# Optimization experiments

Measured on AMD Instinct MI355X. Metric: run time of the kernel, lower is better.

Reference implementation:

```python
import jax, jax.numpy as jnp
import numpy as np

N = 100_000       # nodes
E = 1_600_000     # directed edges (avg degree 16)
IN, H, Z = 128, 128, 64


def setup_inputs() -> dict:
    key = jax.random.key(0)
    ks = jax.random.split(key, 8)
    x = jax.random.normal(ks[0], (N, IN), dtype=jnp.float32)
    edge_index = jax.random.randint(ks[1], (2, E), 0, N, dtype=jnp.int32)
    # Glorot-ish init like PyG GCNConv
    W1 = jax.random.normal(ks[2], (IN, H), dtype=jnp.float32) / np.sqrt(IN).astype(np.float32)
    b1 = jnp.zeros((H,), dtype=jnp.float32)
    Wmu = jax.random.normal(ks[3], (H, Z), dtype=jnp.float32) / np.sqrt(H).astype(np.float32)
    bmu = jnp.zeros((Z,), dtype=jnp.float32)
    Wlv = jax.random.normal(ks[4], (H, Z), dtype=jnp.float32) / np.sqrt(H).astype(np.float32)
    blv = jnp.zeros((Z,), dtype=jnp.float32)
    return {"x": x, "edge_index": edge_index, "W1": W1, "b1": b1,
            "Wmu": Wmu, "bmu": bmu, "Wlv": Wlv, "blv": blv}


def _gcn_conv(x, src, dst, norm, W, b):
    """PyG GCNConv: out = scatter_add(norm * (x @ W)[src], dst) + b."""
    h = x @ W                                   # [N, out_dim]
    msg = h[src] * norm[:, None]                # [E+N, out_dim] gather + scale
    out = jax.ops.segment_sum(msg, dst, num_segments=N)
    return out + b


def reference(x, edge_index, W1, b1, Wmu, bmu, Wlv, blv):
    loop = jnp.arange(N, dtype=edge_index.dtype)
    src = jnp.concatenate([edge_index[0], loop])   # add self-loops (PyG default)
    dst = jnp.concatenate([edge_index[1], loop])
    # symmetric normalization D^{-1/2} (A+I) D^{-1/2}
    deg = jax.ops.segment_sum(jnp.ones_like(dst, dtype=x.dtype), dst, num_segments=N)
    dinv = jax.lax.rsqrt(deg)                      # deg >= 1 thanks to self-loops
    norm = dinv[src] * dinv[dst]                   # [E+N]
    h = jax.nn.relu(_gcn_conv(x, src, dst, norm, W1, b1))
    mu = _gcn_conv(h, src, dst, norm, Wmu, bmu)
    logvar = _gcn_conv(h, src, dst, norm, Wlv, blv)
    return (mu, logvar)
```

## Files before the change

kernel.cpp:

```cpp
#include <hip/hip_runtime.h>
#include <hip/hip_bf16.h>
#include <stdint.h>

static inline size_t ws_align(size_t x) { return (x + 255) & ~(size_t)255; }

typedef __attribute__((ext_vector_type(8))) short bf16x8;
typedef __attribute__((ext_vector_type(4))) float f32x4;

__device__ __forceinline__ uint32_t pack_bf16(float a, float b) {
    uint32_t ua = __float_as_uint(a), ub = __float_as_uint(b);
    ua = (ua + 0x7fffu + ((ua >> 16) & 1u)) >> 16;
    ub = (ub + 0x7fffu + ((ub >> 16) & 1u)) >> 16;
    return ua | (ub << 16);
}
__device__ __forceinline__ uint16_t cvt_bf16(float a) {
    uint32_t ua = __float_as_uint(a);
    return (uint16_t)((ua + 0x7fffu + ((ua >> 16) & 1u)) >> 16);
}
__device__ __forceinline__ float bf_lo(uint32_t v) { return __uint_as_float(v << 16); }
__device__ __forceinline__ float bf_hi(uint32_t v) { return __uint_as_float(v & 0xffff0000u); }


__global__ __launch_bounds__(256) void k_bcount(const int* __restrict__ dst, int* __restrict__ cntAB,
                                                int E, int nchunk, int NB) {
    __shared__ int h[512];
    for (int t = threadIdx.x; t < NB; t += 256) h[t] = 0;
    __syncthreads();
    const int c = blockIdx.x;
    const int per = (E + nchunk - 1) / nchunk;
    const int e0 = c * per, e1 = (e0 + per < E) ? e0 + per : E;
    for (int e = e0 + threadIdx.x; e < e1; e += 256)
        atomicAdd(&h[dst[e] >> 8], 1);
    __syncthreads();
    for (int t = threadIdx.x; t < NB; t += 256) cntAB[t * nchunk + c] = h[t];
}

__global__ __launch_bounds__(256) void k_bscatter(const int* __restrict__ src, const int* __restrict__ dst,
                                                  const int* __restrict__ baseAB, uint2* __restrict__ ebkt,
                                                  int E, int nchunk, int NB) {
    __shared__ int bump[512];
    const int c = blockIdx.x;
    for (int t = threadIdx.x; t < NB; t += 256) bump[t] = baseAB[t * nchunk + c];
    __syncthreads();
    const int per = (E + nchunk - 1) / nchunk;
    const int e0 = c * per, e1 = (e0 + per < E) ? e0 + per : E;
    for (int e = e0 + threadIdx.x; e < e1; e += 256) {
        int d = dst[e], s = src[e];
        int pos = atomicAdd(&bump[d >> 8], 1);
        ebkt[pos] = make_uint2((uint32_t)s, (uint32_t)d);
    }
}

__global__ __launch_bounds__(256) void k_bhist(const uint2* __restrict__ ebkt, const int* __restrict__ baseAB,
                                               int* __restrict__ cnt, int nchunk, int N) {
    __shared__ int h[256];
    h[threadIdx.x] = 0;
    __syncthreads();
    const int b = blockIdx.x;
    const int e0 = baseAB[b * nchunk], e1 = baseAB[(b + 1) * nchunk];
    for (int e = e0 + threadIdx.x; e < e1; e += 256)
        atomicAdd(&h[ebkt[e].y & 255], 1);
    __syncthreads();
    int node = (b << 8) + threadIdx.x;
    if (node < N) cnt[node] = h[threadIdx.x];
}

__global__ __launch_bounds__(256) void k_bfill(const uint2* __restrict__ ebkt, const int* __restrict__ baseAB,
                                               const int* __restrict__ rp, const float* __restrict__ dinv,
                                               uint2* __restrict__ cedge, int nchunk) {
    __shared__ int fl[256];
    fl[threadIdx.x] = 0;
    __syncthreads();
    const int b = blockIdx.x;
    const int e0 = baseAB[b * nchunk], e1 = baseAB[(b + 1) * nchunk];
    for (int e = e0 + threadIdx.x; e < e1; e += 256) {
        uint2 sd = ebkt[e];
        int d = (int)sd.y;
        int posL = atomicAdd(&fl[d & 255], 1);
        cedge[rp[d] + posL] = make_uint2(sd.x, __float_as_uint(dinv[sd.x] * dinv[d]));
    }
}

__global__ void k_dinv(const int* __restrict__ cnt, float* __restrict__ dinv, int N) {
    int i = blockIdx.x * blockDim.x + threadIdx.x;
    if (i < N) dinv[i] = rsqrtf((float)(cnt[i] + 1));
}

__global__ __launch_bounds__(256) void k_scan1(const int* __restrict__ cnt, int* __restrict__ rp,
                                               int* __restrict__ bsum, int N) {
    __shared__ int sh[256];
    int t = threadIdx.x;
    int base = blockIdx.x * 1024 + t * 4;
    int v[4];
#pragma unroll
    for (int i = 0; i < 4; i++) v[i] = (base + i < N) ? cnt[base + i] : 0;
    int s = v[0] + v[1] + v[2] + v[3];
    sh[t] = s;
    __syncthreads();
    for (int off = 1; off < 256; off <<= 1) {
        int x = (t >= off) ? sh[t - off] : 0;
        __syncthreads();
        sh[t] += x;
        __syncthreads();
    }
    int excl = sh[t] - s;
    if (t == 255) bsum[blockIdx.x] = sh[255];
    int run = excl;
#pragma unroll
    for (int i = 0; i < 4; i++) {
        if (base + i < N) rp[base + i] = run;
        run += v[i];
    }
}

__global__ __launch_bounds__(256) void k_scan2(int* __restrict__ bsum, int nb) {
    __shared__ int sh[256];
    int t = threadIdx.x;
    int v = (t < nb) ? bsum[t] : 0;
    sh[t] = v;
    __syncthreads();
    for (int off = 1; off < 256; off <<= 1) {
        int x = (t >= off) ? sh[t - off] : 0;
        __syncthreads();
        sh[t] += x;
        __syncthreads();
    }
    if (t < nb) bsum[t] = sh[t] - v;
}

__global__ void k_scan3(int* __restrict__ rp, const int* __restrict__ bsum, int N, int E) {
    int i = blockIdx.x * blockDim.x + threadIdx.x;
    if (i < N) rp[i] += bsum[i >> 10];
    if (i == N) rp[N] = E;
}

__global__ void k_cvt(const float* __restrict__ in, uint32_t* __restrict__ outp, int n4) {
    int idx = blockIdx.x * blockDim.x + threadIdx.x;
    if (idx >= n4) return;
    float4 v = ((const float4*)in)[idx];
    ((uint2*)outp)[idx] = make_uint2(pack_bf16(v.x, v.y), pack_bf16(v.z, v.w));
}

__global__ __launch_bounds__(256) void k_agg(const uint8_t* __restrict__ featB,
                                             uint32_t* __restrict__ outB,
                                             const int* __restrict__ rp,
                                             const uint2* __restrict__ cedge,
                                             const float* __restrict__ dinv, int N) {
    int node = blockIdx.x * 4 + (threadIdx.x >> 6);
    if (node >= N) return;
    int lane = threadIdx.x & 63;
    const uint32_t off = lane * 4;
    int beg = rp[node], end = rp[node + 1];
    float di = dinv[node];
    float w0 = di * di;
    uint32_t v0 = *(const uint32_t*)(featB + (size_t)node * 256 + off);
    float ax = bf_lo(v0) * w0, ay = bf_hi(v0) * w0;
    int e = beg;
    for (; e + 4 <= end; e += 4) {
        uint2 e0 = cedge[e], e1 = cedge[e + 1], e2 = cedge[e + 2], e3 = cedge[e + 3];
        float wa = __uint_as_float(e0.y), wb = __uint_as_float(e1.y);
        float wc = __uint_as_float(e2.y), wd = __uint_as_float(e3.y);
        uint32_t g0 = *(const uint32_t*)(featB + (size_t)e0.x * 256 + off);
        uint32_t g1 = *(const uint32_t*)(featB + (size_t)e1.x * 256 + off);
        uint32_t g2 = *(const uint32_t*)(featB + (size_t)e2.x * 256 + off);
        uint32_t g3 = *(const uint32_t*)(featB + (size_t)e3.x * 256 + off);
        ax = fmaf(bf_lo(g0), wa, ax); ay = fmaf(bf_hi(g0), wa, ay);
        ax = fmaf(bf_lo(g1), wb, ax); ay = fmaf(bf_hi(g1), wb, ay);
        ax = fmaf(bf_lo(g2), wc, ax); ay = fmaf(bf_hi(g2), wc, ay);
        ax = fmaf(bf_lo(g3), wd, ax); ay = fmaf(bf_hi(g3), wd, ay);
    }
    for (; e < end; ++e) {
        uint2 e0 = cedge[e];
        float wa = __uint_as_float(e0.y);
        uint32_t g0 = *(const uint32_t*)(featB + (size_t)e0.x * 256 + off);
        ax = fmaf(bf_lo(g0), wa, ax); ay = fmaf(bf_hi(g0), wa, ay);
    }
    outB[(size_t)node * 64 + lane] = pack_bf16(ax, ay);
}

__global__ __launch_bounds__(256) void k_gemm1_mfma(
        const uint8_t* __restrict__ A, uint8_t* __restrict__ C,
        const float* __restrict__ W, const float* __restrict__ bias, int N) {
    __shared__ uint32_t Bt[128 * 68];
    {
        int c = threadIdx.x & 127;
        for (int k2 = threadIdx.x >> 7; k2 < 64; k2 += 2)
            Bt[c * 68 + k2] = pack_bf16(W[(2 * k2) * 128 + c], W[(2 * k2 + 1) * 128 + c]);
    }
    __syncthreads();

    const int lane = threadIdx.x & 63;
    const int wv = threadIdx.x >> 6;
    const int rrow = lane & 15;
    const int g = lane >> 4;
    const int r0 = blockIdx.x * 64 + wv * 16;
    const int rl = r0 + rrow;
    const int rc = (rl < N) ? rl : (N - 1);

    bf16x8 a[4];
    const uint8_t* arow = A + (size_t)rc * 256 + g * 16;
#pragma unroll
    for (int kb = 0; kb < 4; kb++) a[kb] = *(const bf16x8*)(arow + kb * 64);

    f32x4 acc[8];
#pragma unroll
    for (int ct = 0; ct < 8; ct++) acc[ct] = (f32x4){0.f, 0.f, 0.f, 0.f};

    const char* btb = (const char*)Bt;
#pragma unroll
    for (int ct = 0; ct < 8; ct++) {
        const char* bp = btb + (ct * 16 + rrow) * 272 + g * 16;
#pragma unroll
        for (int kb = 0; kb < 4; kb++) {
            bf16x8 bfr = *(const bf16x8*)(bp + kb * 64);
            acc[ct] = __builtin_amdgcn_mfma_f32_16x16x32_bf16(a[kb], bfr, acc[ct], 0, 0, 0);
        }
    }

#pragma unroll
    for (int ct = 0; ct < 8; ct++) {
        const int col = ct * 16 + rrow;
        const float bv = bias[col];
#pragma unroll
        for (int r = 0; r < 4; r++) {
            int row = r0 + g * 4 + r;
            if (row < N) {
                float h = fmaxf(acc[ct][r] + bv, 0.f);
                *(uint16_t*)(C + (size_t)row * 256 + col * 2) = cvt_bf16(h);
            }
        }
    }
}

__global__ __launch_bounds__(256) void k_gemm2_mfma(
        const uint8_t* __restrict__ A, float* __restrict__ out,
        const float* __restrict__ Wmu, const float* __restrict__ Wlv,
        const float* __restrict__ bmu, const float* __restrict__ blv, int N) {
    __shared__ uint32_t Bt[128 * 68];
    {
        int c = threadIdx.x & 127;
        const float* Wc = (c < 64) ? (Wmu + c) : (Wlv + (c - 64));
        for (int k2 = threadIdx.x >> 7; k2 < 64; k2 += 2)
            Bt[c * 68 + k2] = pack_bf16(Wc[(2 * k2) * 64], Wc[(2 * k2 + 1) * 64]);
    }
    __syncthreads();

    const int lane = threadIdx.x & 63;
    const int wv = threadIdx.x >> 6;
    const int rrow = lane & 15;
    const int g = lane >> 4;
    const int r0 = blockIdx.x * 64 + wv * 16;
    const int rl = r0 + rrow;
    const int rc = (rl < N) ? rl : (N - 1);

    bf16x8 a[4];
    const uint8_t* arow = A + (size_t)rc * 256 + g * 16;
#pragma unroll
    for (int kb = 0; kb < 4; kb++) a[kb] = *(const bf16x8*)(arow + kb * 64);

    f32x4 acc[8];
#pragma unroll
    for (int ct = 0; ct < 8; ct++) acc[ct] = (f32x4){0.f, 0.f, 0.f, 0.f};

    const char* btb = (const char*)Bt;
#pragma unroll
    for (int ct = 0; ct < 8; ct++) {
        const char* bp = btb + (ct * 16 + rrow) * 272 + g * 16;
#pragma unroll
        for (int kb = 0; kb < 4; kb++) {
            bf16x8 bfr = *(const bf16x8*)(bp + kb * 64);
            acc[ct] = __builtin_amdgcn_mfma_f32_16x16x32_bf16(a[kb], bfr, acc[ct], 0, 0, 0);
        }
    }

#pragma unroll
    for (int ct = 0; ct < 8; ct++) {
        const int col = ct * 16 + rrow;
        const float bv = (col < 64) ? bmu[col] : blv[col - 64];
        float* obase = (col < 64) ? (out + col) : (out + (size_t)N * 64 + (col - 64));
#pragma unroll
        for (int r = 0; r < 4; r++) {
            int row = r0 + g * 4 + r;
            if (row < N) obase[(size_t)row * 64] = acc[ct][r] + bv;
        }
    }
}

extern "C" void kernel_launch(void* const* d_in, const int* in_sizes, int n_in,
                              void* d_out, int out_size, void* d_ws, size_t ws_size,
                              hipStream_t stream) {
    const float* x   = (const float*)d_in[0];
    const int*   ei  = (const int*)d_in[1];
    const float* W1  = (const float*)d_in[2];
    const float* b1  = (const float*)d_in[3];
    const float* Wmu = (const float*)d_in[4];
    const float* bmu = (const float*)d_in[5];
    const float* Wlv = (const float*)d_in[6];
    const float* blv = (const float*)d_in[7];
    float* out = (float*)d_out;

    const int N = in_sizes[0] / 128;
    const int E = in_sizes[1] / 2;
    const int* src = ei;
    const int* dst = ei + E;

    const int nchunk = 256;
    const int NB = (N + 255) >> 8;
    const int M = NB * nchunk;

    char* ws = (char*)d_ws;
    size_t off = 0;
    float* dinv   = (float*)(ws + off); off = ws_align(off + (size_t)N * 4);
    int* cnt      = (int*)(ws + off);   off = ws_align(off + (size_t)N * 4);
    int* rp       = (int*)(ws + off);   off = ws_align(off + (size_t)(N + 1) * 4);
    int* bsum     = (int*)(ws + off);   off = ws_align(off + 1024 * 4);
    int* cntAB    = (int*)(ws + off);   off = ws_align(off + (size_t)(M + 64) * 4);
    int* baseAB   = (int*)(ws + off);   off = ws_align(off + (size_t)(M + 64) * 4);
    uint2* cedge  = (uint2*)(ws + off); off = ws_align(off + (size_t)E * 8);
    uint32_t* xb  = (uint32_t*)(ws + off); off = ws_align(off + (size_t)N * 256);
    uint8_t* F1   = (uint8_t*)(ws + off);  off = ws_align(off + (size_t)N * 256);
    uint2* ebkt   = (uint2*)xb;

    const int b = 256;
    const int nbN = (N + b - 1) / b;

    k_bcount<<<nchunk, 256, 0, stream>>>(dst, cntAB, E, nchunk, NB);
    k_scan1<<<(M + 1023) / 1024, 256, 0, stream>>>(cntAB, baseAB, bsum, M);
    k_scan2<<<1, 256, 0, stream>>>(bsum, (M + 1023) / 1024);
    k_scan3<<<(M + 1 + b - 1) / b, b, 0, stream>>>(baseAB, bsum, M, E);
    k_bscatter<<<nchunk, 256, 0, stream>>>(src, dst, baseAB, ebkt, E, nchunk, NB);
    k_bhist<<<NB, 256, 0, stream>>>(ebkt, baseAB, cnt, nchunk, N);
    k_dinv<<<nbN, b, 0, stream>>>(cnt, dinv, N);
    k_scan1<<<(N + 1023) / 1024, 256, 0, stream>>>(cnt, rp, bsum, N);
    k_scan2<<<1, 256, 0, stream>>>(bsum, (N + 1023) / 1024);
    k_scan3<<<(N + 1 + b - 1) / b, b, 0, stream>>>(rp, bsum, N, E);
    k_bfill<<<NB, 256, 0, stream>>>(ebkt, baseAB, rp, dinv, cedge, nchunk);

    k_cvt<<<(N * 32 + b - 1) / b, b, 0, stream>>>(x, xb, N * 32);
    const int aggBlocks = (N + 3) / 4;
    k_agg<<<aggBlocks, 256, 0, stream>>>((const uint8_t*)xb, (uint32_t*)F1, rp, cedge, dinv, N);
    k_gemm1_mfma<<<(N + 63) / 64, 256, 0, stream>>>(F1, F1, W1, b1, N);

    k_agg<<<aggBlocks, 256, 0, stream>>>(F1, xb, rp, cedge, dinv, N);
    k_gemm2_mfma<<<(N + 63) / 64, 256, 0, stream>>>((const uint8_t*)xb, out, Wmu, Wlv, bmu, blv, N);
}
```

Before: 266.4 us.

## Split aggregation wavefront into four edge groups with 16-byte gathers, fuse dinv into histogram

```diff
diff --git a/kernel.cpp b/kernel.cpp
--- a/kernel.cpp
+++ b/kernel.cpp
@@ -52,7 +52,8 @@
 }
 
 __global__ __launch_bounds__(256) void k_bhist(const uint2* __restrict__ ebkt, const int* __restrict__ baseAB,
-                                               int* __restrict__ cnt, int nchunk, int N) {
+                                               int* __restrict__ cnt, float* __restrict__ dinv,
+                                               int nchunk, int N) {
     __shared__ int h[256];
     h[threadIdx.x] = 0;
     __syncthreads();
@@ -62,7 +63,11 @@
         atomicAdd(&h[ebkt[e].y & 255], 1);
     __syncthreads();
     int node = (b << 8) + threadIdx.x;
-    if (node < N) cnt[node] = h[threadIdx.x];
+    if (node < N) {
+        int c = h[threadIdx.x];
+        cnt[node] = c;
+        dinv[node] = rsqrtf((float)(c + 1));
+    }
 }
 
 __global__ __launch_bounds__(256) void k_bfill(const uint2* __restrict__ ebkt, const int* __restrict__ baseAB,
@@ -79,11 +84,6 @@
         int posL = atomicAdd(&fl[d & 255], 1);
         cedge[rp[d] + posL] = make_uint2(sd.x, __float_as_uint(dinv[sd.x] * dinv[d]));
     }
-}
-
-__global__ void k_dinv(const int* __restrict__ cnt, float* __restrict__ dinv, int N) {
-    int i = blockIdx.x * blockDim.x + threadIdx.x;
-    if (i < N) dinv[i] = rsqrtf((float)(cnt[i] + 1));
 }
 
 __global__ __launch_bounds__(256) void k_scan1(const int* __restrict__ cnt, int* __restrict__ rp,
@@ -149,33 +149,54 @@
     int node = blockIdx.x * 4 + (threadIdx.x >> 6);
     if (node >= N) return;
     int lane = threadIdx.x & 63;
-    const uint32_t off = lane * 4;
+    int j = lane & 15;
+    int q = lane >> 4;
     int beg = rp[node], end = rp[node + 1];
     float di = dinv[node];
-    float w0 = di * di;
-    uint32_t v0 = *(const uint32_t*)(featB + (size_t)node * 256 + off);
-    float ax = bf_lo(v0) * w0, ay = bf_hi(v0) * w0;
-    int e = beg;
-    for (; e + 4 <= end; e += 4) {
-        uint2 e0 = cedge[e], e1 = cedge[e + 1], e2 = cedge[e + 2], e3 = cedge[e + 3];
-        float wa = __uint_as_float(e0.y), wb = __uint_as_float(e1.y);
-        float wc = __uint_as_float(e2.y), wd = __uint_as_float(e3.y);
-        uint32_t g0 = *(const uint32_t*)(featB + (size_t)e0.x * 256 + off);
-        uint32_t g1 = *(const uint32_t*)(featB + (size_t)e1.x * 256 + off);
-        uint32_t g2 = *(const uint32_t*)(featB + (size_t)e2.x * 256 + off);
-        uint32_t g3 = *(const uint32_t*)(featB + (size_t)e3.x * 256 + off);
-        ax = fmaf(bf_lo(g0), wa, ax); ay = fmaf(bf_hi(g0), wa, ay);
-        ax = fmaf(bf_lo(g1), wb, ax); ay = fmaf(bf_hi(g1), wb, ay);
-        ax = fmaf(bf_lo(g2), wc, ax); ay = fmaf(bf_hi(g2), wc, ay);
-        ax = fmaf(bf_lo(g3), wd, ax); ay = fmaf(bf_hi(g3), wd, ay);
-    }
-    for (; e < end; ++e) {
-        uint2 e0 = cedge[e];
-        float wa = __uint_as_float(e0.y);
-        uint32_t g0 = *(const uint32_t*)(featB + (size_t)e0.x * 256 + off);
-        ax = fmaf(bf_lo(g0), wa, ax); ay = fmaf(bf_hi(g0), wa, ay);
-    }
-    outB[(size_t)node * 64 + lane] = pack_bf16(ax, ay);
+    float w0 = (q == 0) ? di * di : 0.0f;
+
+    uint4 sv = *(const uint4*)(featB + (size_t)node * 256 + j * 16);
+    float acc[8];
+    acc[0] = bf_lo(sv.x) * w0; acc[1] = bf_hi(sv.x) * w0;
+    acc[2] = bf_lo(sv.y) * w0; acc[3] = bf_hi(sv.y) * w0;
+    acc[4] = bf_lo(sv.z) * w0; acc[5] = bf_hi(sv.z) * w0;
+    acc[6] = bf_lo(sv.w) * w0; acc[7] = bf_hi(sv.w) * w0;
+
+    int i = beg + q;
+    for (; i + 4 < end; i += 8) {
+        uint2 ea = cedge[i], eb = cedge[i + 4];
+        float wa = __uint_as_float(ea.y), wb = __uint_as_float(eb.y);
+        uint4 ga = *(const uint4*)(featB + (size_t)ea.x * 256 + j * 16);
+        uint4 gb = *(const uint4*)(featB + (size_t)eb.x * 256 + j * 16);
+        acc[0] = fmaf(bf_lo(ga.x), wa, acc[0]); acc[1] = fmaf(bf_hi(ga.x), wa, acc[1]);
+        acc[2] = fmaf(bf_lo(ga.y), wa, acc[2]); acc[3] = fmaf(bf_hi(ga.y), wa, acc[3]);
+        acc[4] = fmaf(bf_lo(ga.z), wa, acc[4]); acc[5] = fmaf(bf_hi(ga.z), wa, acc[5]);
+        acc[6] = fmaf(bf_lo(ga.w), wa, acc[6]); acc[7] = fmaf(bf_hi(ga.w), wa, acc[7]);
+        acc[0] = fmaf(bf_lo(gb.x), wb, acc[0]); acc[1] = fmaf(bf_hi(gb.x), wb, acc[1]);
+        acc[2] = fmaf(bf_lo(gb.y), wb, acc[2]); acc[3] = fmaf(bf_hi(gb.y), wb, acc[3]);
+        acc[4] = fmaf(bf_lo(gb.z), wb, acc[4]); acc[5] = fmaf(bf_hi(gb.z), wb, acc[5]);
+        acc[6] = fmaf(bf_lo(gb.w), wb, acc[6]); acc[7] = fmaf(bf_hi(gb.w), wb, acc[7]);
+    }
+    for (; i < end; i += 4) {
+        uint2 ea = cedge[i];
+        float wa = __uint_as_float(ea.y);
+        uint4 ga = *(const uint4*)(featB + (size_t)ea.x * 256 + j * 16);
+        acc[0] = fmaf(bf_lo(ga.x), wa, acc[0]); acc[1] = fmaf(bf_hi(ga.x), wa, acc[1]);
+        acc[2] = fmaf(bf_lo(ga.y), wa, acc[2]); acc[3] = fmaf(bf_hi(ga.y), wa, acc[3]);
+        acc[4] = fmaf(bf_lo(ga.z), wa, acc[4]); acc[5] = fmaf(bf_hi(ga.z), wa, acc[5]);
+        acc[6] = fmaf(bf_lo(ga.w), wa, acc[6]); acc[7] = fmaf(bf_hi(ga.w), wa, acc[7]);
+    }
+
+#pragma unroll
+    for (int k = 0; k < 8; k++) {
+        acc[k] += __shfl_xor(acc[k], 16, 64);
+        acc[k] += __shfl_xor(acc[k], 32, 64);
+    }
+    if (q == 0) {
+        uint4 p = make_uint4(pack_bf16(acc[0], acc[1]), pack_bf16(acc[2], acc[3]),
+                             pack_bf16(acc[4], acc[5]), pack_bf16(acc[6], acc[7]));
+        *(uint4*)(outB + (size_t)node * 64 + j * 4) = p;
+    }
 }
 
 __global__ __launch_bounds__(256) void k_gemm1_mfma(
@@ -322,15 +343,13 @@
     uint2* ebkt   = (uint2*)xb;
 
     const int b = 256;
-    const int nbN = (N + b - 1) / b;
 
     k_bcount<<<nchunk, 256, 0, stream>>>(dst, cntAB, E, nchunk, NB);
     k_scan1<<<(M + 1023) / 1024, 256, 0, stream>>>(cntAB, baseAB, bsum, M);
     k_scan2<<<1, 256, 0, stream>>>(bsum, (M + 1023) / 1024);
     k_scan3<<<(M + 1 + b - 1) / b, b, 0, stream>>>(baseAB, bsum, M, E);
     k_bscatter<<<nchunk, 256, 0, stream>>>(src, dst, baseAB, ebkt, E, nchunk, NB);
-    k_bhist<<<NB, 256, 0, stream>>>(ebkt, baseAB, cnt, nchunk, N);
-    k_dinv<<<nbN, b, 0, stream>>>(cnt, dinv, N);
+    k_bhist<<<NB, 256, 0, stream>>>(ebkt, baseAB, cnt, dinv, nchunk, N);
     k_scan1<<<(N + 1023) / 1024, 256, 0, stream>>>(cnt, rp, bsum, N);
     k_scan2<<<1, 256, 0, stream>>>(bsum, (N + 1023) / 1024);
     k_scan3<<<(N + 1 + b - 1) / b, b, 0, stream>>>(rp, bsum, N, E);
@@ -341,6 +360,6 @@
     k_agg<<<aggBlocks, 256, 0, stream>>>((const uint8_t*)xb, (uint32_t*)F1, rp, cedge, dinv, N);
     k_gemm1_mfma<<<(N + 63) / 64, 256, 0, stream>>>(F1, F1, W1, b1, N);
 
-    k_agg<<<aggBlocks, 256, 0, stream>>>(F1, xb, rp, cedge, dinv, N);
+    k_agg<<<aggBlocks, 256, 0, stream>>>(F1, (uint32_t*)xb, rp, cedge, dinv, N);
     k_gemm2_mfma<<<(N + 63) / 64, 256, 0, stream>>>((const uint8_t*)xb, out, Wmu, Wlv, bmu, blv, N);
 }
```

Measured after the change: 245.8 us. 7.7% less time.
